# Performance work log

Hardware: AMD Instinct MI355X
Metric: run time of the kernel (lower is better)

Reference implementation:

```python
import jax, jax.numpy as jnp
import numpy as np

N_NODES = 100000
N_EDGES = 1600000
IN_SIZE = 256
OUT_SIZE = 64


def setup_inputs() -> dict:
    key = jax.random.key(0)
    k1, k2, k3 = jax.random.split(key, 3)
    edge_index = jax.random.randint(k1, (2, N_EDGES), 0, N_NODES, dtype=jnp.int32)
    x = jax.random.normal(k2, (N_NODES, IN_SIZE), dtype=jnp.float32)
    W = jax.random.normal(k3, (OUT_SIZE, IN_SIZE), dtype=jnp.float32) * 0.05
    return {"edge_index": edge_index, "x": x, "num_nodes": N_NODES, "W": W}


def reference(edge_index, x, num_nodes, W):
    row, col = edge_index[0], edge_index[1]
    # fill_diag(adj, 1.0): drop any existing diagonal entries (value -> 0),
    # then add exactly one self-loop per node with value 1.0.
    val = jnp.where(row == col, 0.0, 1.0).astype(x.dtype)
    loops = jnp.arange(num_nodes, dtype=row.dtype)
    row_f = jnp.concatenate([row, loops])
    col_f = jnp.concatenate([col, loops])
    val_f = jnp.concatenate([val, jnp.ones((num_nodes,), dtype=x.dtype)])
    # deg = row-sum of adjacency values; D^{-1/2} with inf -> 0
    deg = jax.ops.segment_sum(val_f, row_f, num_segments=num_nodes)
    dinv = jnp.where(deg > 0, deg ** -0.5, 0.0)
    # edge weight: d^{-1/2}[row] * a * d^{-1/2}[col]
    norm = dinv[row_f] * val_f * dinv[col_f]
    # dense projection then SpMM aggregation
    xw = x @ W.T  # [N, out]
    msgs = norm[:, None] * xw[col_f]  # gather over edges [E+N, out]
    out = jax.ops.segment_sum(msgs, row_f, num_segments=num_nodes)
    return out
```

## Files before the change

### kernel.cpp

```cpp
#include <hip/hip_runtime.h>

#define IN_SIZE 256
#define OUT_SIZE 64
#define BSHIFT 7
#define BROWS 128
#define BMASK 127
#define CAP 2560
#define K1_EDGES 4096
#define WPAD 264

typedef __attribute__((ext_vector_type(8))) short short8;
typedef __attribute__((ext_vector_type(4))) float floatx4;

__device__ inline unsigned short f2bf(float f) {
  unsigned u = __builtin_bit_cast(unsigned, f);
  u += 0x7fff + ((u >> 16) & 1);
  return (unsigned short)(u >> 16);
}
__device__ inline float bf2f(unsigned short u) {
  unsigned v = (unsigned)u << 16;
  return __builtin_bit_cast(float, v);
}

__global__ __launch_bounds__(512) void zero_kernel(int* __restrict__ cursor) {
  int i = blockIdx.x * 512 + threadIdx.x;
  if (i < 1024) cursor[i] = 0;
}

struct K1SM {
  union {
    int hist[1024];
    unsigned short w[64 * WPAD];
  };
};

__global__ __launch_bounds__(512) void fused1_kernel(
    const int* __restrict__ row, const int* __restrict__ col,
    int* __restrict__ coarse_cursor, unsigned* __restrict__ pairs,
    const float* __restrict__ x, const float* __restrict__ W,
    unsigned short* __restrict__ xwb, int n_edges, int n_nodes, int nbuck,
    int nb_coarse) {
  __shared__ K1SM sm;
  int tid = threadIdx.x;
  int bid = blockIdx.x;

  if (bid < nb_coarse) {
    sm.hist[tid] = 0;
    sm.hist[tid + 512] = 0;
    __syncthreads();

    int r[8], c[8];
    int ebase = bid * K1_EDGES + tid;
#pragma unroll
    for (int i = 0; i < 8; i++) {
      int e = ebase + i * 512;
      bool ok = e < n_edges;
      r[i] = ok ? row[e] : -1;
      c[i] = ok ? col[e] : -1;
      if (ok && r[i] != c[i]) atomicAdd(&sm.hist[r[i] >> BSHIFT], 1);
    }
    __syncthreads();

    for (int i = tid; i < nbuck; i += 512) {
      int cnt = sm.hist[i];
      if (cnt) sm.hist[i] = atomicAdd(&coarse_cursor[i], cnt);
    }
    __syncthreads();

#pragma unroll
    for (int i = 0; i < 8; i++) {
      if (r[i] >= 0 && r[i] != c[i]) {
        int bin = r[i] >> BSHIFT;
        int slot = atomicAdd(&sm.hist[bin], 1);
        if (slot < CAP)
          pairs[(size_t)bin * CAP + slot] =
              ((unsigned)(r[i] & BMASK) << 17) | (unsigned)c[i];
      }
    }
  } else {
    int mb = bid - nb_coarse;
    long nbase = (long)mb * 128;
    {
      int r = tid >> 3;
      int q = tid & 7;
      const float* src = W + (size_t)r * IN_SIZE + q * 32;
#pragma unroll
      for (int i = 0; i < 4; i++) {
        float4 a = *(const float4*)(src + i * 8);
        float4 b = *(const float4*)(src + i * 8 + 4);
        short8 s;
        s[0] = (short)f2bf(a.x); s[1] = (short)f2bf(a.y);
        s[2] = (short)f2bf(a.z); s[3] = (short)f2bf(a.w);
        s[4] = (short)f2bf(b.x); s[5] = (short)f2bf(b.y);
        s[6] = (short)f2bf(b.z); s[7] = (short)f2bf(b.w);
        *(short8*)(&sm.w[r * WPAD + q * 32 + i * 8]) = s;
      }
    }
    __syncthreads();

    int wave = tid >> 6;
    int lane = tid & 63;
    int quad = lane >> 4;
    int lcol = lane & 15;
    long node = nbase + wave * 16 + lcol;
    long nclamp = (node < (long)n_nodes) ? node : (long)(n_nodes - 1);
    const float* xrow = x + nclamp * IN_SIZE;

    floatx4 acc[4];
#pragma unroll
    for (int t = 0; t < 4; t++) acc[t] = (floatx4){0.f, 0.f, 0.f, 0.f};

#pragma unroll
    for (int kk = 0; kk < 8; kk++) {
      const float* p = xrow + kk * 32 + quad * 8;
      float4 a = *(const float4*)(p);
      float4 bb = *(const float4*)(p + 4);
      short8 bfrag;
      bfrag[0] = (short)f2bf(a.x);  bfrag[1] = (short)f2bf(a.y);
      bfrag[2] = (short)f2bf(a.z);  bfrag[3] = (short)f2bf(a.w);
      bfrag[4] = (short)f2bf(bb.x); bfrag[5] = (short)f2bf(bb.y);
      bfrag[6] = (short)f2bf(bb.z); bfrag[7] = (short)f2bf(bb.w);
#pragma unroll
      for (int t = 0; t < 4; t++) {
        short8 afrag =
            *(const short8*)(&sm.w[(t * 16 + lcol) * WPAD + kk * 32 + quad * 8]);
        acc[t] = __builtin_amdgcn_mfma_f32_16x16x32_bf16(afrag, bfrag, acc[t],
                                                         0, 0, 0);
      }
    }

    if (node < (long)n_nodes) {
#pragma unroll
      for (int t = 0; t < 4; t++) {
        ushort4 sv;
        sv.x = f2bf(acc[t][0]);
        sv.y = f2bf(acc[t][1]);
        sv.z = f2bf(acc[t][2]);
        sv.w = f2bf(acc[t][3]);
        *(ushort4*)(xwb + node * OUT_SIZE + t * 16 + quad * 4) = sv;
      }
    }
  }
}

__global__ __launch_bounds__(512) void fine_kernel(
    const int* __restrict__ coarse_cursor, const unsigned* __restrict__ pairs,
    unsigned* __restrict__ colsp, int* __restrict__ count,
    int* __restrict__ row_start, float* __restrict__ dinv, int n_nodes) {
  __shared__ unsigned lpair[CAP];
  __shared__ int hist[BROWS];
  __shared__ int scn[BROWS];
  int tid = threadIdx.x;
  int b = blockIdx.x;
  size_t base = (size_t)b * CAP;
  int n_b = coarse_cursor[b];
  if (n_b > CAP) n_b = CAP;

  if (tid < BROWS) hist[tid] = 0;
  __syncthreads();

  for (int i = tid; i < n_b; i += 512) {
    unsigned p = pairs[base + i];
    lpair[i] = p;
    atomicAdd(&hist[p >> 17], 1);
  }
  __syncthreads();

  if (tid < BROWS) scn[tid] = hist[tid];
  __syncthreads();
  for (int off = 1; off < BROWS; off <<= 1) {
    int t = (tid >= off && tid < BROWS) ? scn[tid - off] : 0;
    __syncthreads();
    if (tid < BROWS) scn[tid] += t;
    __syncthreads();
  }

  if (tid < BROWS) {
    int e = (tid > 0) ? scn[tid - 1] : 0;
    int r = b * BROWS + tid;
    if (r < n_nodes) {
      int deg = hist[tid];
      count[r] = deg;
      row_start[r] = (int)base + e;
      dinv[r] = rsqrtf((float)deg + 1.0f);
    }
    hist[tid] = e;
  }
  __syncthreads();

  for (int i = tid; i < n_b; i += 512) {
    unsigned p = lpair[i];
    int slot = atomicAdd(&hist[p >> 17], 1);
    colsp[base + slot] = p & 0x1FFFFu;
  }
}

__global__ __launch_bounds__(256) void gather_kernel(
    const int* __restrict__ row_start, const int* __restrict__ count,
    const unsigned* __restrict__ colsp, const float* __restrict__ dinv,
    const unsigned short* __restrict__ xwb, float* __restrict__ out,
    int n_nodes) {
  int lane = threadIdx.x & 63;
  int wave = threadIdx.x >> 6;
  int sub = lane & 7;
  int cg = lane >> 3;
  int rb = (blockIdx.x * 4 + wave) * 4;
  if (rb >= n_nodes) return;

  int start[4], cnt[4];
  int maxc = 0;
#pragma unroll
  for (int i = 0; i < 4; i++) {
    int r = rb + i;
    bool ok = r < n_nodes;
    start[i] = ok ? row_start[r] : 0;
    cnt[i] = ok ? count[r] : 0;
    maxc = max(maxc, cnt[i]);
  }

  float acc[4][8];
#pragma unroll
  for (int i = 0; i < 4; i++)
#pragma unroll
    for (int k = 0; k < 8; k++) acc[i][k] = 0.f;

  if (sub == 0) {
#pragma unroll
    for (int i = 0; i < 4; i++) {
      int r = rb + i;
      if (r < n_nodes) {
        float dv = dinv[r];
        short8 v = *(const short8*)(xwb + (size_t)r * OUT_SIZE + cg * 8);
#pragma unroll
        for (int k = 0; k < 8; k++) acc[i][k] = dv * bf2f((unsigned short)v[k]);
      }
    }
  }

  for (int j = 0; j < maxc; j += 8) {
    int c[4];
    float m[4];
    int idx = j + sub;
#pragma unroll
    for (int i = 0; i < 4; i++) {
      bool act = idx < cnt[i];
      c[i] = act ? (int)colsp[start[i] + idx] : rb;
      m[i] = act ? dinv[c[i]] : 0.0f;
    }
    short8 v[4];
#pragma unroll
    for (int i = 0; i < 4; i++)
      v[i] = *(const short8*)(xwb + (size_t)c[i] * OUT_SIZE + cg * 8);
#pragma unroll
    for (int i = 0; i < 4; i++)
#pragma unroll
      for (int k = 0; k < 8; k++)
        acc[i][k] += m[i] * bf2f((unsigned short)v[i][k]);
  }

#pragma unroll
  for (int i = 0; i < 4; i++)
#pragma unroll
    for (int k = 0; k < 8; k++) {
      acc[i][k] += __shfl_xor(acc[i][k], 1);
      acc[i][k] += __shfl_xor(acc[i][k], 2);
      acc[i][k] += __shfl_xor(acc[i][k], 4);
    }

  if (sub == 0) {
#pragma unroll
    for (int i = 0; i < 4; i++) {
      int r = rb + i;
      if (r < n_nodes) {
        float dr = dinv[r];
        float* dst = out + (size_t)r * OUT_SIZE + cg * 8;
        *(float4*)(dst) =
            make_float4(dr * acc[i][0], dr * acc[i][1], dr * acc[i][2],
                        dr * acc[i][3]);
        *(float4*)(dst + 4) =
            make_float4(dr * acc[i][4], dr * acc[i][5], dr * acc[i][6],
                        dr * acc[i][7]);
      }
    }
  }
}

extern "C" void kernel_launch(void* const* d_in, const int* in_sizes, int n_in,
                              void* d_out, int out_size, void* d_ws,
                              size_t ws_size, hipStream_t stream) {
  const int* edge_index = (const int*)d_in[0];
  const float* x = (const float*)d_in[1];
  const float* W = (const float*)d_in[3];

  int n_edges = in_sizes[0] / 2;
  int n_nodes = in_sizes[1] / IN_SIZE;
  const int* row = edge_index;
  const int* col = edge_index + n_edges;
  float* out = (float*)d_out;

  int nbuck = (n_nodes + BROWS - 1) >> BSHIFT;
  int nb_coarse = (n_edges + K1_EDGES - 1) / K1_EDGES;
  int nb_mm = (n_nodes + 127) / 128;

  char* ws = (char*)d_ws;
  size_t nb4 = ((size_t)n_nodes * 4 + 15) & ~(size_t)15;
  int* count = (int*)ws;
  int* row_start = (int*)(ws + nb4);
  float* dinv = (float*)(ws + 2 * nb4);
  int* coarse_cursor = (int*)(ws + 3 * nb4);
  size_t pairsB = (size_t)nbuck * CAP * 4;
  unsigned* pairs = (unsigned*)(ws + 3 * nb4 + 4096);
  unsigned* colsp = (unsigned*)(ws + 3 * nb4 + 4096 + pairsB);
  unsigned short* xwb =
      (unsigned short*)(ws + 3 * nb4 + 4096 + 2 * pairsB);

  zero_kernel<<<2, 512, 0, stream>>>(coarse_cursor);
  fused1_kernel<<<nb_coarse + nb_mm, 512, 0, stream>>>(
      row, col, coarse_cursor, pairs, x, W, xwb, n_edges, n_nodes, nbuck,
      nb_coarse);
  fine_kernel<<<nbuck, 512, 0, stream>>>(coarse_cursor, pairs, colsp, count,
                                         row_start, dinv, n_nodes);
  gather_kernel<<<(n_nodes + 15) / 16, 256, 0, stream>>>(
      row_start, count, colsp, dinv, xwb, out, n_nodes);
}
```

Baseline: 254.6 us.

## Pre-convert W to bf16 once and read it from global instead of LDS

The zero kernel becomes a prep kernel that also converts W to bf16 into workspace. The fused kernel then drops its large LDS W tile and per-block conversion, reading A fragments straight from global/L2, which shrinks shared memory to the histogram. Block size drops from 512 to 256, with edge blocks processing 16 edges per thread and matmul blocks covering 64 nodes. This aims to raise occupancy and remove redundant W conversion per block, at the cost of uncoalesced global/L2 reads for W fragments.

Result: slower. 264.5 us (+3.9%).

```diff
diff --git a/kernel.cpp b/kernel.cpp
--- a/kernel.cpp
+++ b/kernel.cpp
@@ -7,7 +7,7 @@
 #define BMASK 127
 #define CAP 2560
 #define K1_EDGES 4096
-#define WPAD 264
+#define MMROWS 64
 
 typedef __attribute__((ext_vector_type(8))) short short8;
 typedef __attribute__((ext_vector_type(4))) float floatx4;
@@ -22,56 +22,52 @@
   return __builtin_bit_cast(float, v);
 }
 
-__global__ __launch_bounds__(512) void zero_kernel(int* __restrict__ cursor) {
-  int i = blockIdx.x * 512 + threadIdx.x;
+__global__ __launch_bounds__(256) void prep_kernel(const float* __restrict__ W,
+                                                   unsigned short* __restrict__ Wb,
+                                                   int* __restrict__ cursor) {
+  int i = blockIdx.x * 256 + threadIdx.x;
+  if (i < OUT_SIZE * IN_SIZE) Wb[i] = f2bf(W[i]);
   if (i < 1024) cursor[i] = 0;
 }
 
-struct K1SM {
-  union {
-    int hist[1024];
-    unsigned short w[64 * WPAD];
-  };
-};
-
-__global__ __launch_bounds__(512) void fused1_kernel(
+__global__ __launch_bounds__(256) void fused1_kernel(
     const int* __restrict__ row, const int* __restrict__ col,
     int* __restrict__ coarse_cursor, unsigned* __restrict__ pairs,
-    const float* __restrict__ x, const float* __restrict__ W,
+    const float* __restrict__ x, const unsigned short* __restrict__ Wb,
     unsigned short* __restrict__ xwb, int n_edges, int n_nodes, int nbuck,
     int nb_coarse) {
-  __shared__ K1SM sm;
+  __shared__ int hist[1024];
   int tid = threadIdx.x;
   int bid = blockIdx.x;
 
   if (bid < nb_coarse) {
-    sm.hist[tid] = 0;
-    sm.hist[tid + 512] = 0;
-    __syncthreads();
-
-    int r[8], c[8];
+#pragma unroll
+    for (int i = 0; i < 4; i++) hist[tid + i * 256] = 0;
+    __syncthreads();
+
+    int r[16], c[16];
     int ebase = bid * K1_EDGES + tid;
 #pragma unroll
-    for (int i = 0; i < 8; i++) {
-      int e = ebase + i * 512;
+    for (int i = 0; i < 16; i++) {
+      int e = ebase + i * 256;
       bool ok = e < n_edges;
       r[i] = ok ? row[e] : -1;
       c[i] = ok ? col[e] : -1;
-      if (ok && r[i] != c[i]) atomicAdd(&sm.hist[r[i] >> BSHIFT], 1);
-    }
-    __syncthreads();
-
-    for (int i = tid; i < nbuck; i += 512) {
-      int cnt = sm.hist[i];
-      if (cnt) sm.hist[i] = atomicAdd(&coarse_cursor[i], cnt);
-    }
-    __syncthreads();
-
-#pragma unroll
-    for (int i = 0; i < 8; i++) {
+      if (ok && r[i] != c[i]) atomicAdd(&hist[r[i] >> BSHIFT], 1);
+    }
+    __syncthreads();
+
+    for (int i = tid; i < nbuck; i += 256) {
+      int cnt = hist[i];
+      if (cnt) hist[i] = atomicAdd(&coarse_cursor[i], cnt);
+    }
+    __syncthreads();
+
+#pragma unroll
+    for (int i = 0; i < 16; i++) {
       if (r[i] >= 0 && r[i] != c[i]) {
         int bin = r[i] >> BSHIFT;
-        int slot = atomicAdd(&sm.hist[bin], 1);
+        int slot = atomicAdd(&hist[bin], 1);
         if (slot < CAP)
           pairs[(size_t)bin * CAP + slot] =
               ((unsigned)(r[i] & BMASK) << 17) | (unsigned)c[i];
@@ -79,30 +75,11 @@
     }
   } else {
     int mb = bid - nb_coarse;
-    long nbase = (long)mb * 128;
-    {
-      int r = tid >> 3;
-      int q = tid & 7;
-      const float* src = W + (size_t)r * IN_SIZE + q * 32;
-#pragma unroll
-      for (int i = 0; i < 4; i++) {
-        float4 a = *(const float4*)(src + i * 8);
-        float4 b = *(const float4*)(src + i * 8 + 4);
-        short8 s;
-        s[0] = (short)f2bf(a.x); s[1] = (short)f2bf(a.y);
-        s[2] = (short)f2bf(a.z); s[3] = (short)f2bf(a.w);
-        s[4] = (short)f2bf(b.x); s[5] = (short)f2bf(b.y);
-        s[6] = (short)f2bf(b.z); s[7] = (short)f2bf(b.w);
-        *(short8*)(&sm.w[r * WPAD + q * 32 + i * 8]) = s;
-      }
-    }
-    __syncthreads();
-
     int wave = tid >> 6;
     int lane = tid & 63;
     int quad = lane >> 4;
     int lcol = lane & 15;
-    long node = nbase + wave * 16 + lcol;
+    long node = (long)mb * MMROWS + wave * 16 + lcol;
     long nclamp = (node < (long)n_nodes) ? node : (long)(n_nodes - 1);
     const float* xrow = x + nclamp * IN_SIZE;
 
@@ -122,8 +99,8 @@
       bfrag[6] = (short)f2bf(bb.z); bfrag[7] = (short)f2bf(bb.w);
 #pragma unroll
       for (int t = 0; t < 4; t++) {
-        short8 afrag =
-            *(const short8*)(&sm.w[(t * 16 + lcol) * WPAD + kk * 32 + quad * 8]);
+        short8 afrag = *(const short8*)(
+            Wb + (size_t)(t * 16 + lcol) * IN_SIZE + kk * 32 + quad * 8);
         acc[t] = __builtin_amdgcn_mfma_f32_16x16x32_bf16(afrag, bfrag, acc[t],
                                                          0, 0, 0);
       }
@@ -300,7 +277,7 @@
 
   int nbuck = (n_nodes + BROWS - 1) >> BSHIFT;
   int nb_coarse = (n_edges + K1_EDGES - 1) / K1_EDGES;
-  int nb_mm = (n_nodes + 127) / 128;
+  int nb_mm = (n_nodes + MMROWS - 1) / MMROWS;
 
   char* ws = (char*)d_ws;
   size_t nb4 = ((size_t)n_nodes * 4 + 15) & ~(size_t)15;
@@ -313,10 +290,14 @@
   unsigned* colsp = (unsigned*)(ws + 3 * nb4 + 4096 + pairsB);
   unsigned short* xwb =
       (unsigned short*)(ws + 3 * nb4 + 4096 + 2 * pairsB);
-
-  zero_kernel<<<2, 512, 0, stream>>>(coarse_cursor);
-  fused1_kernel<<<nb_coarse + nb_mm, 512, 0, stream>>>(
-      row, col, coarse_cursor, pairs, x, W, xwb, n_edges, n_nodes, nbuck,
+  unsigned short* Wb =
+      (unsigned short*)(ws + 3 * nb4 + 4096 + 2 * pairsB +
+                        (size_t)n_nodes * OUT_SIZE * 2);
+
+  prep_kernel<<<(OUT_SIZE * IN_SIZE + 255) / 256, 256, 0, stream>>>(
+      W, Wb, coarse_cursor);
+  fused1_kernel<<<nb_coarse + nb_mm, 256, 0, stream>>>(
+      row, col, coarse_cursor, pairs, x, Wb, xwb, n_edges, n_nodes, nbuck,
       nb_coarse);
   fine_kernel<<<nbuck, 512, 0, stream>>>(coarse_cursor, pairs, colsp, count,
                                          row_start, dinv, n_nodes);
```
